# Performance work log

Hardware: AMD Instinct MI355X
Metric: run time of the kernel (lower is better)

The kernel has to match this reference:

```python
import jax, jax.numpy as jnp
import numpy as np

N, E, DIM, H = 100000, 1600000, 128, 8
HD = DIM // H  # head_dim


def setup_inputs() -> dict:
    key = jax.random.key(0)
    ks = jax.random.split(key, 12)
    s = lambda k, sh, fan: jax.random.normal(k, sh, jnp.float32) * (1.0 / np.sqrt(fan))
    return {
        "x": jax.random.normal(ks[0], (N, DIM), jnp.float32),
        "src": jax.random.randint(ks[1], (E,), 0, N, jnp.int32),
        "dst": jax.random.randint(ks[2], (E,), 0, N, jnp.int32),
        # input_linear: dim -> dim
        "w_in": s(ks[3], (DIM, DIM), DIM), "b_in": jnp.zeros((DIM,), jnp.float32),
        # attn_linear_u: dim -> H (with bias); attn_linear_v: dim -> H (no bias)
        "w_au": s(ks[4], (DIM, H), DIM), "b_au": jnp.zeros((H,), jnp.float32),
        "w_av": s(ks[5], (DIM, H), DIM),
        # feed-forward: dim -> dim (hidden_dim_multiplier=1) -> dim
        "w1": s(ks[6], (DIM, DIM), DIM), "b1": jnp.zeros((DIM,), jnp.float32),
        "w2": s(ks[7], (DIM, DIM), DIM), "b2": jnpp if False else jnp.zeros((DIM,), jnp.float32),
    }


def reference(x, src, dst, w_in, b_in, w_au, b_au, w_av, w1, b1, w2, b2):
    n = x.shape[0]
    h = x @ w_in + b_in                      # [N, dim]
    a_u = h @ w_au + b_au                    # [N, H]
    a_v = h @ w_av                           # [N, H]
    # u_add_v: per-edge scores, then LeakyReLU(0.2)
    scores = jax.nn.leaky_relu(a_u[src] + a_v[dst], negative_slope=0.2)  # [E, H]
    # edge_softmax: normalize over incoming edges of each dst node
    smax = jax.ops.segment_max(scores, dst, num_segments=n)              # [N, H]
    ex = jnp.exp(scores - smax[dst])                                     # [E, H]
    denom = jax.ops.segment_sum(ex, dst, num_segments=n)                 # [N, H]
    probs = ex / denom[dst]                                              # [E, H]
    # u_mul_e_sum with x reshaped to [N, head_dim, H]
    hv = h.reshape(n, HD, H)
    msg = hv[src] * probs[:, None, :]                                    # [E, HD, H]
    agg = jax.ops.segment_sum(msg, dst, num_segments=n)                  # [N, HD, H]
    out = agg.reshape(n, DIM)
    # feed-forward (dropout=0, eval)
    out = jax.nn.gelu(out @ w1 + b1) @ w2 + b2
    return out
```

## Files before the change

kernel.cpp:

```cpp
#include <hip/hip_runtime.h>
#include <hip/hip_bf16.h>
#include <stdint.h>

#define DIM 128
#define NH 8
#define CH 4096
#define BK 128
#define LS 136
#define EBUF 4096

using bf16 = __hip_bfloat16;
typedef __attribute__((ext_vector_type(8))) short short8;
typedef __attribute__((ext_vector_type(4))) float floatx4;


__device__ inline float bf2f(unsigned short b) {
    return __uint_as_float(((unsigned)b) << 16);
}
__device__ inline unsigned short f2bf(float f) {
    unsigned u = __float_as_uint(f);
    u += 0x7FFFu + ((u >> 16) & 1u);
    return (unsigned short)(u >> 16);
}

__device__ inline float gelu_tanh(float x) {
    float x3 = x * x * x;
    float u = 0.7978845608028654f * (x + 0.044715f * x3);
    float e = __expf(2.f * u);
    float t = 1.f - 2.f / (e + 1.f);
    return 0.5f * x * (1.f + t);
}

__launch_bounds__(256)
__global__ void scatter_pre_kernel(const int* __restrict__ src, const int* __restrict__ dst,
                                   int* __restrict__ lofs, int* __restrict__ mat,
                                   unsigned* __restrict__ packed, int* __restrict__ total,
                                   int E, int K, int B,
                                   const float* __restrict__ w_in, const float* __restrict__ w1,
                                   const float* __restrict__ w2, const float* __restrict__ w_au,
                                   const float* __restrict__ w_av,
                                   unsigned short* __restrict__ w_in_b, unsigned short* __restrict__ w1_b,
                                   unsigned short* __restrict__ w2_b, unsigned short* __restrict__ wc_b) {
    __shared__ int hist[1024];
    __shared__ int cur[1024];
    __shared__ int wsum[4];
    const int b = blockIdx.x, tid = threadIdx.x;
    if (b < B) {
        for (int k = tid; k < 1024; k += 256) hist[k] = 0;
        __syncthreads();
        const int base = b * CH, end = min(base + CH, E);
        for (int i = base + tid; i < end; i += 256)
            atomicAdd(&hist[dst[i] >> 7], 1);
        __syncthreads();
        int v[4]; int t = 0;
        #pragma unroll
        for (int j = 0; j < 4; ++j) { int x = hist[tid * 4 + j]; v[j] = t; t += x; }
        const int lane = tid & 63, wv = tid >> 6;
        int incl = t;
        #pragma unroll
        for (int off = 1; off < 64; off <<= 1) {
            int y = __shfl_up(incl, off);
            if (lane >= off) incl += y;
        }
        if (lane == 63) wsum[wv] = incl;
        __syncthreads();
        int woff = 0;
        #pragma unroll
        for (int w = 0; w < 4; ++w) if (w < wv) woff += wsum[w];
        int texcl = woff + incl - t;
        #pragma unroll
        for (int j = 0; j < 4; ++j) {
            int k = tid * 4 + j;
            int e = texcl + v[j];
            cur[k] = e;
            if (k < K) {
                lofs[(size_t)b * K + k] = e;
                mat[(size_t)b * 1024 + k] = hist[k];
            }
        }
        __syncthreads();
        for (int i = base + tid; i < end; i += 256) {
            int d = dst[i], s = src[i];
            int pos = atomicAdd(&cur[d >> 7], 1);
            packed[(size_t)b * CH + pos] = (unsigned)s | ((unsigned)(d & 127) << 20);
        }
    } else {
        int pb = b - B;
        if (pb < 12) {
            const int m = pb >> 2, qtr = pb & 3;
            const float* W = m == 0 ? w_in : (m == 1 ? w1 : w2);
            unsigned short* O = m == 0 ? w_in_b : (m == 1 ? w1_b : w2_b);
            const bool perm = (m == 1);
            #pragma unroll
            for (int i = 0; i < 16; ++i) {
                int o = qtr * 4096 + tid + i * 256;
                int k = o & 127, n = o >> 7;
                int krow = perm ? ((k & 15) * 8 + (k >> 4)) : k;
                O[o] = f2bf(W[krow * 128 + n]);
            }
        } else {
            #pragma unroll
            for (int i = 0; i < 8; ++i) {
                int o = tid + i * 256;
                int j = o >> 7, kt = o & 127;
                int ko = (kt & 15) * 8 + (kt >> 4);
                float v = (j < 8) ? w_au[ko * 8 + j] : w_av[ko * 8 + (j - 8)];
                wc_b[o] = f2bf(v);
            }
            if (tid == 0) total[0] = 0;
        }
    }
}

__device__ __forceinline__ void stage_pre(unsigned short* wt, const unsigned short* __restrict__ pre,
                                          int tid) {
    #pragma unroll
    for (int i = 0; i < 4; ++i) {
        int g = tid + i * 512;
        short8 v = *(const short8*)(pre + g * 8);
        *(short8*)(wt + (g >> 4) * LS + (g & 15) * 8) = v;
    }
}

__launch_bounds__(512)
__global__ void gia_scan_kernel(const float* __restrict__ x, const unsigned short* __restrict__ w_in_b,
                                const float* __restrict__ b_in,
                                const unsigned short* __restrict__ wc_b, const float* __restrict__ b_au,
                                bf16* __restrict__ h, float* __restrict__ au,
                                float* __restrict__ av, int M, int RB,
                                const int* __restrict__ mat, int* __restrict__ matx,
                                int* __restrict__ btot, int* __restrict__ bbase,
                                int* __restrict__ total, int K, int B) {
    __shared__ __align__(16) unsigned short wt[128 * LS];
    __shared__ __align__(16) unsigned short wc[16 * LS];
    __shared__ int sscr[8];
    const int tid = threadIdx.x;

    if ((int)blockIdx.x >= RB) {
        const int k = blockIdx.x - RB;
        int v = (tid < B) ? mat[(size_t)tid * 1024 + k] : 0;
        const int lane = tid & 63, wv = tid >> 6;
        int incl = v;
        #pragma unroll
        for (int off = 1; off < 64; off <<= 1) {
            int y = __shfl_up(incl, off);
            if (lane >= off) incl += y;
        }
        if (lane == 63) sscr[wv] = incl;
        __syncthreads();
        int woff = 0, tot = 0;
        #pragma unroll
        for (int w = 0; w < 8; ++w) { int s = sscr[w]; if (w < wv) woff += s; tot += s; }
        if (tid < B) matx[(size_t)k * B + tid] = woff + incl - v;
        if (tid == 0) { bbase[k] = atomicAdd(total, tot); btot[k] = tot; }
        return;
    }

    stage_pre(wt, w_in_b, tid);
    {
        int j = tid >> 5, kt4 = (tid & 31) * 4;
        const unsigned* s = (const unsigned*)(wc_b + j * 128 + kt4);
        unsigned* d = (unsigned*)(wc + j * LS + kt4);
        d[0] = s[0]; d[1] = s[1];
    }
    __syncthreads();

    const int wave = tid >> 6;
    const int lane = tid & 63;
    const int l15 = lane & 15;
    const int q = lane >> 4;
    const int rowbase = blockIdx.x * 128 + wave * 16;
    const int rowA = min(rowbase + l15, M - 1);

    floatx4 acc[8];
    #pragma unroll
    for (int c = 0; c < 8; ++c) acc[c] = (floatx4){0.f, 0.f, 0.f, 0.f};

    #pragma unroll
    for (int kk = 0; kk < 4; ++kk) {
        const float* ap = x + (size_t)rowA * 128 + kk * 32 + q * 8;
        floatx4 a0 = *(const floatx4*)ap;
        floatx4 a1 = *(const floatx4*)(ap + 4);
        union { short8 s; unsigned short u[8]; } cv;
        #pragma unroll
        for (int j = 0; j < 4; ++j) { cv.u[j] = f2bf(a0[j]); cv.u[4 + j] = f2bf(a1[j]); }
        short8 afrag = cv.s;
        #pragma unroll
        for (int c = 0; c < 8; ++c) {
            short8 bfrag = *(const short8*)(wt + (c * 16 + l15) * LS + kk * 32 + q * 8);
            acc[c] = __builtin_amdgcn_mfma_f32_16x16x32_bf16(afrag, bfrag, acc[c], 0, 0, 0);
        }
    }
    __syncthreads();

    const int rl0 = wave * 16 + q * 4;
    #pragma unroll
    for (int c = 0; c < 8; ++c) {
        int col = c * 16 + l15;
        int colw = (col & 7) * 16 + (col >> 3);
        float b = b_in[col];
        #pragma unroll
        for (int r = 0; r < 4; ++r)
            wt[(rl0 + r) * LS + colw] = f2bf(acc[c][r] + b);
    }
    __syncthreads();

    const int blk0 = blockIdx.x * 128;
    #pragma unroll
    for (int i = 0; i < 4; ++i) {
        int g = tid + i * 512;
        int row = g >> 4;
        if (blk0 + row < M) {
            short8 v = *(const short8*)(wt + row * LS + (g & 15) * 8);
            *(short8*)((unsigned short*)h + (size_t)(blk0 + row) * 128 + (g & 15) * 8) = v;
        }
    }

    floatx4 acc2 = (floatx4){0.f, 0.f, 0.f, 0.f};
    #pragma unroll
    for (int kk = 0; kk < 4; ++kk) {
        short8 af = *(const short8*)(wt + (wave * 16 + l15) * LS + kk * 32 + q * 8);
        short8 bf = *(const short8*)(wc + l15 * LS + kk * 32 + q * 8);
        acc2 = __builtin_amdgcn_mfma_f32_16x16x32_bf16(af, bf, acc2, 0, 0, 0);
    }
    {
        const int row0 = rowbase + q * 4;
        int col = l15;
        #pragma unroll
        for (int r = 0; r < 4; ++r) {
            int rr = row0 + r;
            if (rr < M) {
                if (col < 8) au[(size_t)rr * 8 + col] = acc2[r] + b_au[col];
                else         av[(size_t)rr * 8 + (col - 8)] = acc2[r];
            }
        }
    }
}

__launch_bounds__(512)
__global__ void ff_kernel(const bf16* __restrict__ A, const unsigned short* __restrict__ w1_b,
                          const float* __restrict__ b1, const unsigned short* __restrict__ w2_b,
                          const float* __restrict__ b2, float* __restrict__ out, int M) {
    __shared__ __align__(16) unsigned short wt[128 * LS];
    __shared__ __align__(16) unsigned short ht[128 * LS];
    const int tid = threadIdx.x;

    stage_pre(wt, w1_b, tid);
    __syncthreads();

    const int wave = tid >> 6;
    const int lane = tid & 63;
    const int l15 = lane & 15;
    const int q = lane >> 4;
    const int rowbase = blockIdx.x * 128 + wave * 16;
    const int rowA = min(rowbase + l15, M - 1);

    floatx4 acc[8];
    #pragma unroll
    for (int c = 0; c < 8; ++c) acc[c] = (floatx4){0.f, 0.f, 0.f, 0.f};

    #pragma unroll
    for (int kk = 0; kk < 4; ++kk) {
        short8 afrag = *(const short8*)((const unsigned short*)A + (size_t)rowA * 128 + kk * 32 + q * 8);
        #pragma unroll
        for (int c = 0; c < 8; ++c) {
            short8 bfrag = *(const short8*)(wt + (c * 16 + l15) * LS + kk * 32 + q * 8);
            acc[c] = __builtin_amdgcn_mfma_f32_16x16x32_bf16(afrag, bfrag, acc[c], 0, 0, 0);
        }
    }
    __syncthreads();

    stage_pre(wt, w2_b, tid);
    const int rl0 = wave * 16 + q * 4;
    #pragma unroll
    for (int c = 0; c < 8; ++c) {
        int col = c * 16 + l15;
        float b = b1[col];
        #pragma unroll
        for (int r = 0; r < 4; ++r)
            ht[(rl0 + r) * LS + col] = f2bf(gelu_tanh(acc[c][r] + b));
    }
    __syncthreads();

    floatx4 acc2[8];
    #pragma unroll
    for (int c = 0; c < 8; ++c) acc2[c] = (floatx4){0.f, 0.f, 0.f, 0.f};
    #pragma unroll
    for (int kk = 0; kk < 4; ++kk) {
        short8 af = *(const short8*)(ht + (wave * 16 + l15) * LS + kk * 32 + q * 8);
        #pragma unroll
        for (int c = 0; c < 8; ++c) {
            short8 bfrag = *(const short8*)(wt + (c * 16 + l15) * LS + kk * 32 + q * 8);
            acc2[c] = __builtin_amdgcn_mfma_f32_16x16x32_bf16(af, bfrag, acc2[c], 0, 0, 0);
        }
    }

    const int row0 = rowbase + q * 4;
    #pragma unroll
    for (int c = 0; c < 8; ++c) {
        int col = c * 16 + l15;
        float b = b2[col];
        #pragma unroll
        for (int r = 0; r < 4; ++r) {
            int rr = row0 + r;
            if (rr < M) out[(size_t)rr * 128 + col] = acc2[c][r] + b;
        }
    }
}

__launch_bounds__(256)
__global__ void bucket_csr_kernel(const unsigned* __restrict__ packed, const int* __restrict__ lofs,
                                  const int* __restrict__ matx,
                                  const int* __restrict__ bbase, const int* __restrict__ btot,
                                  int* __restrict__ rowptr, int* __restrict__ deg,
                                  int* __restrict__ esrc, int N, int E, int K, int B) {
    __shared__ unsigned ebuf[EBUF];
    __shared__ int hist[128], cur[128];
    __shared__ int wtot;
    const int k = blockIdx.x, tid = threadIdx.x;
    const int start = bbase[k];
    const int cnt = btot[k];

    for (int b = tid; b < B; b += 256) {
        int lo = lofs[(size_t)b * K + k];
        int chunk_len = min(CH, E - b * CH);
        int hi = (k + 1 < K) ? lofs[(size_t)b * K + k + 1] : chunk_len;
        int dbase = matx[(size_t)k * B + b];
        const unsigned* sp = packed + (size_t)b * CH;
        for (int j = lo; j < hi; ++j) ebuf[dbase + (j - lo)] = sp[j];
    }
    if (tid < 128) hist[tid] = 0;
    __syncthreads();

    for (int i = tid; i < cnt; i += 256)
        atomicAdd(&hist[ebuf[i] >> 20], 1);
    __syncthreads();

    const int lane = tid & 63;
    int v = (tid < 128) ? hist[tid] : 0;
    int incl = v;
    #pragma unroll
    for (int off = 1; off < 64; off <<= 1) {
        int y = __shfl_up(incl, off);
        if (lane >= off) incl += y;
    }
    if (tid == 63) wtot = incl;
    __syncthreads();
    int excl = incl - v + ((tid >= 64 && tid < 128) ? wtot : 0);
    if (tid < 128) {
        int n = k * BK + tid;
        if (n < N) { rowptr[n] = start + excl; deg[n] = v; }
        cur[tid] = excl;
    }
    __syncthreads();

    for (int i = tid; i < cnt; i += 256) {
        unsigned p = ebuf[i];
        int pos = atomicAdd(&cur[p >> 20], 1);
        esrc[start + pos] = (int)(p & 0xFFFFFu);
    }
}


__device__ __forceinline__ void unpack8fma(uint4 w, float p, float* o) {
    o[0] = fmaf(p, __uint_as_float(w.x << 16), o[0]);
    o[1] = fmaf(p, __uint_as_float(w.x & 0xFFFF0000u), o[1]);
    o[2] = fmaf(p, __uint_as_float(w.y << 16), o[2]);
    o[3] = fmaf(p, __uint_as_float(w.y & 0xFFFF0000u), o[3]);
    o[4] = fmaf(p, __uint_as_float(w.z << 16), o[4]);
    o[5] = fmaf(p, __uint_as_float(w.z & 0xFFFF0000u), o[5]);
    o[6] = fmaf(p, __uint_as_float(w.w << 16), o[6]);
    o[7] = fmaf(p, __uint_as_float(w.w & 0xFFFF0000u), o[7]);
}

template <bool MASKED>
__device__ __forceinline__ void do8e(const int* __restrict__ ep, int i, int nd,
                                     int e, int head, int d0b,
                                     const float* __restrict__ au,
                                     const char* __restrict__ hpb,
                                     float avh, float& l, float* o) {
    int idx = i + e;
    int s;
    float m = 1.f;
    if constexpr (MASKED) {
        s = ep[min(idx, nd - 1)];
        m = idx < nd ? 1.f : 0.f;
    } else {
        s = ep[idx];
    }
    float a = au[(s << 3) + head];
    size_t off = ((size_t)(unsigned)s) << 8;
    uint4 w0 = *(const uint4*)(hpb + off + d0b);
    uint4 w1 = *(const uint4*)(hpb + off + d0b + 16);
    float x = a + avh;
    x = fmaxf(x, 0.2f * x);
    float p = __expf(x);
    if constexpr (MASKED) p *= m;
    l += p;
    unpack8fma(w0, p, o);
    unpack8fma(w1, p, o + 8);
}

__launch_bounds__(256)
__global__ void agg_csr_kernel(const int* __restrict__ rowptr, const int* __restrict__ deg,
                               const int* __restrict__ esrc,
                               const float* __restrict__ au, const float* __restrict__ av,
                               const bf16* __restrict__ h, bf16* __restrict__ agg, int N) {
    const int node = (blockIdx.x * 256 + threadIdx.x) >> 6;
    if (node >= N) return;
    const int lane = threadIdx.x & 63;
    const int e = lane >> 3;
    const int head = lane & 7;
    const int d0b = head * 32;
    const char* hpb = (const char*)h;
    const int nd = deg[node];
    const int start = rowptr[node];
    const float avh = av[((size_t)node << 3) + head];
    const int* ep = esrc + start;

    float l0 = 0.f;
    float o[16];
    #pragma unroll
    for (int j = 0; j < 16; ++j) o[j] = 0.f;

    int i = 0;
    for (; i + 16 <= nd; i += 16) {
        do8e<false>(ep, i, nd, e, head, d0b, au, hpb, avh, l0, o);
        do8e<false>(ep, i + 8, nd, e, head, d0b, au, hpb, avh, l0, o);
    }
    if (i + 8 <= nd) { do8e<false>(ep, i, nd, e, head, d0b, au, hpb, avh, l0, o); i += 8; }
    if (i < nd) do8e<true>(ep, i, nd, e, head, d0b, au, hpb, avh, l0, o);

    #pragma unroll
    for (int j = 0; j < 16; ++j) {
        o[j] += __shfl_xor(o[j], 8);
        o[j] += __shfl_xor(o[j], 16);
        o[j] += __shfl_xor(o[j], 32);
    }
    l0 += __shfl_xor(l0, 8);
    l0 += __shfl_xor(l0, 16);
    l0 += __shfl_xor(l0, 32);

    if (lane < 8) {
        float inv = l0 > 0.f ? 1.f / l0 : 0.f;
        unsigned r[8];
        #pragma unroll
        for (int j = 0; j < 8; ++j)
            r[j] = ((unsigned)f2bf(o[2 * j + 1] * inv) << 16) | (unsigned)f2bf(o[2 * j] * inv);
        char* outp = (char*)agg + ((size_t)node << 8) + lane * 32;
        *(uint4*)outp = (uint4){r[0], r[1], r[2], r[3]};
        *(uint4*)(outp + 16) = (uint4){r[4], r[5], r[6], r[7]};
    }
}

extern "C" void kernel_launch(void* const* d_in, const int* in_sizes, int n_in,
                              void* d_out, int out_size, void* d_ws, size_t ws_size,
                              hipStream_t stream) {
    const float* x    = (const float*)d_in[0];
    const int*   src  = (const int*)d_in[1];
    const int*   dst  = (const int*)d_in[2];
    const float* w_in = (const float*)d_in[3];
    const float* b_in = (const float*)d_in[4];
    const float* w_au = (const float*)d_in[5];
    const float* b_au = (const float*)d_in[6];
    const float* w_av = (const float*)d_in[7];
    const float* w1   = (const float*)d_in[8];
    const float* b1   = (const float*)d_in[9];
    const float* w2   = (const float*)d_in[10];
    const float* b2   = (const float*)d_in[11];
    const int N = in_sizes[0] / DIM;
    const int E = in_sizes[1];
    const int K = (N + BK - 1) / BK;
    const int B = (E + CH - 1) / CH;

    char* p = (char*)d_ws;
    int*  deg    = (int*)p;  p += (size_t)N * 4;
    int*  rowptr = (int*)p;  p += (size_t)N * 4;
    int*  esrc   = (int*)p;  p += (size_t)E * 4;
    bf16* h      = (bf16*)p; p += (size_t)N * DIM * 2;
    float* au    = (float*)p; p += (size_t)N * NH * 4;
    float* av    = (float*)p; p += (size_t)N * NH * 4;
    unsigned short* w_in_b = (unsigned short*)p; p += 128 * 128 * 2;
    unsigned short* w1_b   = (unsigned short*)p; p += 128 * 128 * 2;
    unsigned short* w2_b   = (unsigned short*)p; p += 128 * 128 * 2;
    unsigned short* wc_b   = (unsigned short*)p; p += 16 * 128 * 2;
    int* total = (int*)p; p += 64;
    bf16* agg    = (bf16*)p;  p += (size_t)N * DIM * 2;
    unsigned* packed = (unsigned*)agg;
    int* mat   = (int*)((char*)agg + (size_t)B * CH * 4);
    int* matx  = mat + (size_t)B * 1024;
    int* btot  = matx + (size_t)K * B;
    int* bbase = btot + K;
    int* lofs  = bbase + K;

    const int row_blocks = (N + 127) / 128;

    scatter_pre_kernel<<<B + 13, 256, 0, stream>>>(src, dst, lofs, mat, packed, total,
                                                   E, K, B, w_in, w1, w2, w_au, w_av,
                                                   w_in_b, w1_b, w2_b, wc_b);

    gia_scan_kernel<<<row_blocks + K, 512, 0, stream>>>(x, w_in_b, b_in, wc_b, b_au,
                                                        h, au, av, N, row_blocks,
                                                        mat, matx, btot, bbase, total, K, B);

    bucket_csr_kernel<<<K, 256, 0, stream>>>(packed, lofs, matx, bbase, btot,
                                             rowptr, deg, esrc, N, E, K, B);

    agg_csr_kernel<<<(N + 3) / 4, 256, 0, stream>>>(rowptr, deg, esrc, au, av, h, agg, N);

    ff_kernel<<<row_blocks, 512, 0, stream>>>(agg, w1_b, b1, w2_b, b2, (float*)d_out, N);
}
```

Before: 278.8 us.

## Fuse bucket CSR build into aggregation kernel using LDS-resident edge lists

```diff
diff --git a/kernel.cpp b/kernel.cpp
--- a/kernel.cpp
+++ b/kernel.cpp
@@ -33,8 +33,7 @@
 
 __launch_bounds__(256)
 __global__ void scatter_pre_kernel(const int* __restrict__ src, const int* __restrict__ dst,
-                                   int* __restrict__ lofs, int* __restrict__ mat,
-                                   unsigned* __restrict__ packed, int* __restrict__ total,
+                                   int* __restrict__ lofs, unsigned* __restrict__ packed,
                                    int E, int K, int B,
                                    const float* __restrict__ w_in, const float* __restrict__ w1,
                                    const float* __restrict__ w2, const float* __restrict__ w_au,
@@ -73,10 +72,7 @@
             int k = tid * 4 + j;
             int e = texcl + v[j];
             cur[k] = e;
-            if (k < K) {
-                lofs[(size_t)b * K + k] = e;
-                mat[(size_t)b * 1024 + k] = hist[k];
-            }
+            if (k < K) lofs[(size_t)b * K + k] = e;
         }
         __syncthreads();
         for (int i = base + tid; i < end; i += 256) {
@@ -107,7 +103,6 @@
                 float v = (j < 8) ? w_au[ko * 8 + j] : w_av[ko * 8 + (j - 8)];
                 wc_b[o] = f2bf(v);
             }
-            if (tid == 0) total[0] = 0;
         }
     }
 }
@@ -123,38 +118,14 @@
 }
 
 __launch_bounds__(512)
-__global__ void gia_scan_kernel(const float* __restrict__ x, const unsigned short* __restrict__ w_in_b,
-                                const float* __restrict__ b_in,
-                                const unsigned short* __restrict__ wc_b, const float* __restrict__ b_au,
-                                bf16* __restrict__ h, float* __restrict__ au,
-                                float* __restrict__ av, int M, int RB,
-                                const int* __restrict__ mat, int* __restrict__ matx,
-                                int* __restrict__ btot, int* __restrict__ bbase,
-                                int* __restrict__ total, int K, int B) {
+__global__ void gemm_in_attn_kernel(const float* __restrict__ x, const unsigned short* __restrict__ w_in_b,
+                                    const float* __restrict__ b_in,
+                                    const unsigned short* __restrict__ wc_b, const float* __restrict__ b_au,
+                                    bf16* __restrict__ h, float* __restrict__ au,
+                                    float* __restrict__ av, int M) {
     __shared__ __align__(16) unsigned short wt[128 * LS];
     __shared__ __align__(16) unsigned short wc[16 * LS];
-    __shared__ int sscr[8];
     const int tid = threadIdx.x;
-
-    if ((int)blockIdx.x >= RB) {
-        const int k = blockIdx.x - RB;
-        int v = (tid < B) ? mat[(size_t)tid * 1024 + k] : 0;
-        const int lane = tid & 63, wv = tid >> 6;
-        int incl = v;
-        #pragma unroll
-        for (int off = 1; off < 64; off <<= 1) {
-            int y = __shfl_up(incl, off);
-            if (lane >= off) incl += y;
-        }
-        if (lane == 63) sscr[wv] = incl;
-        __syncthreads();
-        int woff = 0, tot = 0;
-        #pragma unroll
-        for (int w = 0; w < 8; ++w) { int s = sscr[w]; if (w < wv) woff += s; tot += s; }
-        if (tid < B) matx[(size_t)k * B + tid] = woff + incl - v;
-        if (tid == 0) { bbase[k] = atomicAdd(total, tot); btot[k] = tot; }
-        return;
-    }
 
     stage_pre(wt, w_in_b, tid);
     {
@@ -305,59 +276,6 @@
             int rr = row0 + r;
             if (rr < M) out[(size_t)rr * 128 + col] = acc2[c][r] + b;
         }
-    }
-}
-
-__launch_bounds__(256)
-__global__ void bucket_csr_kernel(const unsigned* __restrict__ packed, const int* __restrict__ lofs,
-                                  const int* __restrict__ matx,
-                                  const int* __restrict__ bbase, const int* __restrict__ btot,
-                                  int* __restrict__ rowptr, int* __restrict__ deg,
-                                  int* __restrict__ esrc, int N, int E, int K, int B) {
-    __shared__ unsigned ebuf[EBUF];
-    __shared__ int hist[128], cur[128];
-    __shared__ int wtot;
-    const int k = blockIdx.x, tid = threadIdx.x;
-    const int start = bbase[k];
-    const int cnt = btot[k];
-
-    for (int b = tid; b < B; b += 256) {
-        int lo = lofs[(size_t)b * K + k];
-        int chunk_len = min(CH, E - b * CH);
-        int hi = (k + 1 < K) ? lofs[(size_t)b * K + k + 1] : chunk_len;
-        int dbase = matx[(size_t)k * B + b];
-        const unsigned* sp = packed + (size_t)b * CH;
-        for (int j = lo; j < hi; ++j) ebuf[dbase + (j - lo)] = sp[j];
-    }
-    if (tid < 128) hist[tid] = 0;
-    __syncthreads();
-
-    for (int i = tid; i < cnt; i += 256)
-        atomicAdd(&hist[ebuf[i] >> 20], 1);
-    __syncthreads();
-
-    const int lane = tid & 63;
-    int v = (tid < 128) ? hist[tid] : 0;
-    int incl = v;
-    #pragma unroll
-    for (int off = 1; off < 64; off <<= 1) {
-        int y = __shfl_up(incl, off);
-        if (lane >= off) incl += y;
-    }
-    if (tid == 63) wtot = incl;
-    __syncthreads();
-    int excl = incl - v + ((tid >= 64 && tid < 128) ? wtot : 0);
-    if (tid < 128) {
-        int n = k * BK + tid;
-        if (n < N) { rowptr[n] = start + excl; deg[n] = v; }
-        cur[tid] = excl;
-    }
-    __syncthreads();
-
-    for (int i = tid; i < cnt; i += 256) {
-        unsigned p = ebuf[i];
-        int pos = atomicAdd(&cur[p >> 20], 1);
-        esrc[start + pos] = (int)(p & 0xFFFFFu);
     }
 }
 
@@ -374,19 +292,19 @@
 }
 
 template <bool MASKED>
-__device__ __forceinline__ void do8e(const int* __restrict__ ep, int i, int nd,
-                                     int e, int head, int d0b,
-                                     const float* __restrict__ au,
-                                     const char* __restrict__ hpb,
-                                     float avh, float& l, float* o) {
+__device__ __forceinline__ void do8e_lds(const unsigned* ep, int i, int nd,
+                                         int e, int head, int d0b,
+                                         const float* __restrict__ au,
+                                         const char* __restrict__ hpb,
+                                         float avh, float& l, float* o) {
     int idx = i + e;
     int s;
     float m = 1.f;
     if constexpr (MASKED) {
-        s = ep[min(idx, nd - 1)];
+        s = (int)ep[min(idx, nd - 1)];
         m = idx < nd ? 1.f : 0.f;
     } else {
-        s = ep[idx];
+        s = (int)ep[idx];
     }
     float a = au[(s << 3) + head];
     size_t off = ((size_t)(unsigned)s) << 8;
@@ -401,55 +319,122 @@
     unpack8fma(w1, p, o + 8);
 }
 
-__launch_bounds__(256)
-__global__ void agg_csr_kernel(const int* __restrict__ rowptr, const int* __restrict__ deg,
-                               const int* __restrict__ esrc,
+__launch_bounds__(512)
+__global__ void csr_agg_kernel(const unsigned* __restrict__ packed, const int* __restrict__ lofs,
                                const float* __restrict__ au, const float* __restrict__ av,
-                               const bf16* __restrict__ h, bf16* __restrict__ agg, int N) {
-    const int node = (blockIdx.x * 256 + threadIdx.x) >> 6;
-    if (node >= N) return;
-    const int lane = threadIdx.x & 63;
+                               const bf16* __restrict__ h, bf16* __restrict__ agg,
+                               int N, int E, int K, int B) {
+    __shared__ unsigned ebuf[EBUF];
+    __shared__ unsigned ebuf2[EBUF];
+    __shared__ int dsc[512];
+    __shared__ int hist[128], cur[128], rpl[128];
+    __shared__ int wsum[8];
+    __shared__ int wtot;
+    const int k = blockIdx.x, tid = threadIdx.x;
+    const int lane = tid & 63, wv = tid >> 6;
+
+    int lo = 0, hi = 0;
+    if (tid < B) {
+        lo = lofs[(size_t)tid * K + k];
+        int chunk_len = min(CH, E - tid * CH);
+        hi = (k + 1 < K) ? lofs[(size_t)tid * K + (k + 1)] : chunk_len;
+    }
+    int len = hi - lo;
+    if (tid < 128) hist[tid] = 0;
+    int incl = len;
+    #pragma unroll
+    for (int off = 1; off < 64; off <<= 1) {
+        int y = __shfl_up(incl, off);
+        if (lane >= off) incl += y;
+    }
+    if (lane == 63) wsum[wv] = incl;
+    __syncthreads();
+    int woff = 0, cnt = 0;
+    #pragma unroll
+    for (int w = 0; w < 8; ++w) { int s = wsum[w]; if (w < wv) woff += s; cnt += s; }
+    if (tid < B) dsc[tid] = woff + incl - len;
+    __syncthreads();
+
+    for (int b = tid; b < B; b += 512) {
+        int blo = lofs[(size_t)b * K + k];
+        int chunk_len = min(CH, E - b * CH);
+        int bhi = (k + 1 < K) ? lofs[(size_t)b * K + (k + 1)] : chunk_len;
+        int dbase = dsc[b];
+        const unsigned* sp = packed + (size_t)b * CH;
+        for (int j = blo; j < bhi; ++j) ebuf[dbase + (j - blo)] = sp[j];
+    }
+    __syncthreads();
+
+    for (int i = tid; i < cnt; i += 512)
+        atomicAdd(&hist[ebuf[i] >> 20], 1);
+    __syncthreads();
+
+    int v = (tid < 128) ? hist[tid] : 0;
+    int incl2 = v;
+    #pragma unroll
+    for (int off = 1; off < 64; off <<= 1) {
+        int y = __shfl_up(incl2, off);
+        if (lane >= off) incl2 += y;
+    }
+    if (tid == 63) wtot = incl2;
+    __syncthreads();
+    int excl = incl2 - v + ((tid >= 64 && tid < 128) ? wtot : 0);
+    if (tid < 128) { rpl[tid] = excl; cur[tid] = excl; }
+    __syncthreads();
+
+    for (int i = tid; i < cnt; i += 512) {
+        unsigned p = ebuf[i];
+        int pos = atomicAdd(&cur[p >> 20], 1);
+        ebuf2[pos] = p & 0xFFFFFu;
+    }
+    __syncthreads();
+
     const int e = lane >> 3;
     const int head = lane & 7;
     const int d0b = head * 32;
     const char* hpb = (const char*)h;
-    const int nd = deg[node];
-    const int start = rowptr[node];
-    const float avh = av[((size_t)node << 3) + head];
-    const int* ep = esrc + start;
-
-    float l0 = 0.f;
-    float o[16];
-    #pragma unroll
-    for (int j = 0; j < 16; ++j) o[j] = 0.f;
-
-    int i = 0;
-    for (; i + 16 <= nd; i += 16) {
-        do8e<false>(ep, i, nd, e, head, d0b, au, hpb, avh, l0, o);
-        do8e<false>(ep, i + 8, nd, e, head, d0b, au, hpb, avh, l0, o);
-    }
-    if (i + 8 <= nd) { do8e<false>(ep, i, nd, e, head, d0b, au, hpb, avh, l0, o); i += 8; }
-    if (i < nd) do8e<true>(ep, i, nd, e, head, d0b, au, hpb, avh, l0, o);
-
-    #pragma unroll
-    for (int j = 0; j < 16; ++j) {
-        o[j] += __shfl_xor(o[j], 8);
-        o[j] += __shfl_xor(o[j], 16);
-        o[j] += __shfl_xor(o[j], 32);
-    }
-    l0 += __shfl_xor(l0, 8);
-    l0 += __shfl_xor(l0, 16);
-    l0 += __shfl_xor(l0, 32);
-
-    if (lane < 8) {
-        float inv = l0 > 0.f ? 1.f / l0 : 0.f;
-        unsigned r[8];
-        #pragma unroll
-        for (int j = 0; j < 8; ++j)
-            r[j] = ((unsigned)f2bf(o[2 * j + 1] * inv) << 16) | (unsigned)f2bf(o[2 * j] * inv);
-        char* outp = (char*)agg + ((size_t)node << 8) + lane * 32;
-        *(uint4*)outp = (uint4){r[0], r[1], r[2], r[3]};
-        *(uint4*)(outp + 16) = (uint4){r[4], r[5], r[6], r[7]};
+
+    for (int t = 0; t < 16; ++t) {
+        int nl = wv * 16 + t;
+        int node = k * BK + nl;
+        if (node >= N) break;
+        const int nd = hist[nl];
+        const unsigned* ep = ebuf2 + rpl[nl];
+        const float avh = av[((size_t)node << 3) + head];
+
+        float l0 = 0.f;
+        float o[16];
+        #pragma unroll
+        for (int j = 0; j < 16; ++j) o[j] = 0.f;
+
+        int i = 0;
+        for (; i + 16 <= nd; i += 16) {
+            do8e_lds<false>(ep, i, nd, e, head, d0b, au, hpb, avh, l0, o);
+            do8e_lds<false>(ep, i + 8, nd, e, head, d0b, au, hpb, avh, l0, o);
+        }
+        if (i + 8 <= nd) { do8e_lds<false>(ep, i, nd, e, head, d0b, au, hpb, avh, l0, o); i += 8; }
+        if (i < nd) do8e_lds<true>(ep, i, nd, e, head, d0b, au, hpb, avh, l0, o);
+
+        #pragma unroll
+        for (int j = 0; j < 16; ++j) {
+            o[j] += __shfl_xor(o[j], 8);
+            o[j] += __shfl_xor(o[j], 16);
+            o[j] += __shfl_xor(o[j], 32);
+        }
+        l0 += __shfl_xor(l0, 8);
+        l0 += __shfl_xor(l0, 16);
+        l0 += __shfl_xor(l0, 32);
+
+        if (lane < 8) {
+            float inv = l0 > 0.f ? 1.f / l0 : 0.f;
+            unsigned r[8];
+            #pragma unroll
+            for (int j = 0; j < 8; ++j)
+                r[j] = ((unsigned)f2bf(o[2 * j + 1] * inv) << 16) | (unsigned)f2bf(o[2 * j] * inv);
+            char* outp = (char*)agg + ((size_t)node << 8) + lane * 32;
+            *(uint4*)outp = (uint4){r[0], r[1], r[2], r[3]};
+            *(uint4*)(outp + 16) = (uint4){r[4], r[5], r[6], r[7]};
+        }
     }
 }
 
@@ -474,39 +459,27 @@
     const int B = (E + CH - 1) / CH;
 
     char* p = (char*)d_ws;
-    int*  deg    = (int*)p;  p += (size_t)N * 4;
-    int*  rowptr = (int*)p;  p += (size_t)N * 4;
-    int*  esrc   = (int*)p;  p += (size_t)E * 4;
     bf16* h      = (bf16*)p; p += (size_t)N * DIM * 2;
     float* au    = (float*)p; p += (size_t)N * NH * 4;
     float* av    = (float*)p; p += (size_t)N * NH * 4;
+    bf16* agg    = (bf16*)p; p += (size_t)N * DIM * 2;
+    unsigned* packed = (unsigned*)p; p += (size_t)B * CH * 4;
+    int* lofs  = (int*)p; p += (size_t)B * K * 4;
     unsigned short* w_in_b = (unsigned short*)p; p += 128 * 128 * 2;
     unsigned short* w1_b   = (unsigned short*)p; p += 128 * 128 * 2;
     unsigned short* w2_b   = (unsigned short*)p; p += 128 * 128 * 2;
     unsigned short* wc_b   = (unsigned short*)p; p += 16 * 128 * 2;
-    int* total = (int*)p; p += 64;
-    bf16* agg    = (bf16*)p;  p += (size_t)N * DIM * 2;
-    unsigned* packed = (unsigned*)agg;
-    int* mat   = (int*)((char*)agg + (size_t)B * CH * 4);
-    int* matx  = mat + (size_t)B * 1024;
-    int* btot  = matx + (size_t)K * B;
-    int* bbase = btot + K;
-    int* lofs  = bbase + K;
 
     const int row_blocks = (N + 127) / 128;
 
-    scatter_pre_kernel<<<B + 13, 256, 0, stream>>>(src, dst, lofs, mat, packed, total,
+    scatter_pre_kernel<<<B + 13, 256, 0, stream>>>(src, dst, lofs, packed,
                                                    E, K, B, w_in, w1, w2, w_au, w_av,
                                                    w_in_b, w1_b, w2_b, wc_b);
 
-    gia_scan_kernel<<<row_blocks + K, 512, 0, stream>>>(x, w_in_b, b_in, wc_b, b_au,
-                                                        h, au, av, N, row_blocks,
-                                                        mat, matx, btot, bbase, total, K, B);
-
-    bucket_csr_kernel<<<K, 256, 0, stream>>>(packed, lofs, matx, bbase, btot,
-                                             rowptr, deg, esrc, N, E, K, B);
-
-    agg_csr_kernel<<<(N + 3) / 4, 256, 0, stream>>>(rowptr, deg, esrc, au, av, h, agg, N);
+    gemm_in_attn_kernel<<<row_blocks, 512, 0, stream>>>(x, w_in_b, b_in, wc_b, b_au,
+                                                        h, au, av, N);
+
+    csr_agg_kernel<<<K, 512, 0, stream>>>(packed, lofs, au, av, h, agg, N, E, K, B);
 
     ff_kernel<<<row_blocks, 512, 0, stream>>>(agg, w1_b, b1, w2_b, b2, (float*)d_out, N);
 }
```

After: 285.2 us. +2.3%, slower.
